# Kernel tuning notes

Measured on AMD Instinct MI355X. Metric: run time of the kernel, lower is better.

## Reference

```python
import jax, jax.numpy as jnp
import numpy as np

B, H, S, D = 2, 16, 2048, 64


def setup_inputs() -> dict:
    key = jax.random.key(0)
    kq, kk, kv = jax.random.split(key, 3)
    q = jax.random.normal(kq, (B, H, S, D), dtype=jnp.float32)
    k = jax.random.normal(kk, (B, H, S, D), dtype=jnp.float32)
    v = jax.random.normal(kv, (B, H, S, D), dtype=jnp.float32)
    # causal mask: 1.0 where attention is DISALLOWED (strictly upper triangle)
    mask = jnp.triu(jnp.ones((S, S), dtype=jnp.float32), k=1)[None, None, :, :]
    return {"k": k, "q": q, "v": v, "mask": mask}


def reference(k, q, v, mask):
    d_k = jnp.asarray(k.shape[-1], dtype=jnp.float32)
    # scores: [B, H, S, S]
    scores = jnp.einsum("bhqd,bhkd->bhqk", q, k) / jnp.sqrt(d_k)
    scores = scores + mask * (-1e9)
    weights = jax.nn.softmax(scores, axis=-1)
    # attention output: [B, H, S, D]
    return jnp.einsum("bhqk,bhkd->bhqd", weights, v)
```

## Files before the change

kernel.cpp:

```cpp
#include <hip/hip_runtime.h>
#include <hip/hip_bf16.h>

typedef unsigned short ushort_t;
typedef __attribute__((ext_vector_type(8))) short v8s;
typedef __attribute__((ext_vector_type(4))) float v4f;

#define SEQ   2048
#define DH    64
#define NHEAD 32
#define BK    32
#define NQT32 64
#define KSTR  72
#define VSTR  40

__device__ __forceinline__ unsigned pkbf(float lo, float hi) {
    __hip_bfloat162 h = __float22bfloat162_rn(make_float2(lo, hi));
    union { __hip_bfloat162 h; unsigned u; } c; c.h = h; return c.u;
}

__device__ __forceinline__ v8s load8_bf_scaled(const float* p, float sc) {
    float4 a = *(const float4*)p;
    float4 b = *(const float4*)(p + 4);
    union { v8s v; unsigned u[4]; } t;
    t.u[0] = pkbf(a.x * sc, a.y * sc);
    t.u[1] = pkbf(a.z * sc, a.w * sc);
    t.u[2] = pkbf(b.x * sc, b.y * sc);
    t.u[3] = pkbf(b.z * sc, b.w * sc);
    return t.v;
}

__device__ __forceinline__ void stage_store(ushort_t* kdst, ushort_t* vdst,
                                            float4 k0, float4 k1,
                                            const float* va, const float* vb) {
    union { v8s v; unsigned u[4]; } kc, vc;
    kc.u[0] = pkbf(k0.x, k0.y); kc.u[1] = pkbf(k0.z, k0.w);
    kc.u[2] = pkbf(k1.x, k1.y); kc.u[3] = pkbf(k1.z, k1.w);
    vc.u[0] = pkbf(va[0], vb[0]); vc.u[1] = pkbf(va[1], vb[1]);
    vc.u[2] = pkbf(va[2], vb[2]); vc.u[3] = pkbf(va[3], vb[3]);
    *(v8s*)kdst = kc.v;
    *(v8s*)vdst = vc.v;
}

__global__ __launch_bounds__(256, 4)
void attn_causal_kernel(const float* __restrict__ Kg,
                        const float* __restrict__ Qg,
                        const float* __restrict__ Vg,
                        float* __restrict__ Og) {
    __shared__ alignas(16) ushort_t Kt[2][BK * KSTR];
    __shared__ alignas(16) ushort_t Vt[2][DH * VSTR];
    __shared__ alignas(16) ushort_t Pb[4][16 * VSTR];

    const int i    = blockIdx.x;
    const int head = i & 31;
    const int pair = i >> 5;
    const int qbL  = pair * 32;
    const int qbH  = (NQT32 - 1 - pair) * 32;
    const int tid  = threadIdx.x;
    const int wv   = tid >> 6;
    const int lane = tid & 63;
    const int l15  = lane & 15;
    const int quad = lane >> 4;

    const int myq0 = (wv < 2) ? (qbL + wv * 16) : (qbH + (wv - 2) * 16);
    const int qmax = myq0 + 15;

    const size_t hb = (size_t)head * SEQ * DH;

    v8s qa0, qa1;
    {
        const float* qp = Qg + hb + (size_t)(myq0 + l15) * DH + quad * 8;
        qa0 = load8_bf_scaled(qp, 0.125f);
        qa1 = load8_bf_scaled(qp + 32, 0.125f);
    }

    v4f a0 = {0.f,0.f,0.f,0.f}, a1 = a0, a2 = a0, a3 = a0;
    float lsum[4] = {0.f,0.f,0.f,0.f};

    const int ntiles = NQT32 - pair;

    const int sk_kpos = tid >> 3;
    const int sk_d    = (tid & 7) * 8;
    const int sv_d = tid & 63;

    const float* kbase  = Kg + hb + (size_t)sk_kpos * DH + sk_d;
    const float* vbaseA = Vg + hb + (size_t)(4 * wv) * DH + sv_d;
    const float* vbaseB = Vg + hb + (size_t)(16 + 4 * wv) * DH + sv_d;
    ushort_t* kdst0 = &Kt[0][sk_kpos * KSTR + sk_d];
    ushort_t* vdst0 = &Vt[0][sv_d * VSTR + wv * 8];
    const int kofs = BK * KSTR;
    const int vofs = DH * VSTR;

    {
        float4 k0 = *(const float4*)(kbase);
        float4 k1 = *(const float4*)(kbase + 4);
        float va[4], vb[4];
        #pragma unroll
        for (int m = 0; m < 4; ++m) {
            va[m] = vbaseA[(size_t)m * DH];
            vb[m] = vbaseB[(size_t)m * DH];
        }
        stage_store(kdst0, vdst0, k0, k1, va, vb);
    }
    __syncthreads();

    for (int kt = 0; kt < ntiles; ++kt) {
        const int cur = kt & 1;
        const bool havenext = (kt + 1 < ntiles);

        float4 nk0, nk1; float nva[4], nvb[4];
        if (havenext) {
            const size_t toff = (size_t)(kt + 1) * BK * DH;
            nk0 = *(const float4*)(kbase + toff);
            nk1 = *(const float4*)(kbase + toff + 4);
            #pragma unroll
            for (int m = 0; m < 4; ++m) {
                nva[m] = vbaseA[toff + (size_t)m * DH];
                nvb[m] = vbaseB[toff + (size_t)m * DH];
            }
        }

        const int kb = kt * BK;
        if (kb <= qmax) {
            const ushort_t* KB = &Kt[0][cur ? kofs : 0];
            const ushort_t* VB = &Vt[0][cur ? vofs : 0];
            union { v8s v; uint4 u; } k00, k01, k10, k11, vb0, vb1, vb2, vb3;
            k00.u = *(const uint4*)&KB[(l15)      * KSTR      + quad * 8];
            k01.u = *(const uint4*)&KB[(l15)      * KSTR + 32 + quad * 8];
            k10.u = *(const uint4*)&KB[(16 + l15) * KSTR      + quad * 8];
            k11.u = *(const uint4*)&KB[(16 + l15) * KSTR + 32 + quad * 8];
            vb0.u = *(const uint4*)&VB[(l15)      * VSTR + quad * 8];
            vb1.u = *(const uint4*)&VB[(16 + l15) * VSTR + quad * 8];
            vb2.u = *(const uint4*)&VB[(32 + l15) * VSTR + quad * 8];
            vb3.u = *(const uint4*)&VB[(48 + l15) * VSTR + quad * 8];

            const v4f z = {0.f, 0.f, 0.f, 0.f};
            v4f c0 = __builtin_amdgcn_mfma_f32_16x16x32_bf16(qa0, k00.v, z, 0, 0, 0);
            c0     = __builtin_amdgcn_mfma_f32_16x16x32_bf16(qa1, k01.v, c0, 0, 0, 0);
            v4f c1 = __builtin_amdgcn_mfma_f32_16x16x32_bf16(qa0, k10.v, z, 0, 0, 0);
            c1     = __builtin_amdgcn_mfma_f32_16x16x32_bf16(qa1, k11.v, c1, 0, 0, 0);

            float p0[4], p1[4];
            if (kb + BK <= myq0) {
                #pragma unroll
                for (int r = 0; r < 4; ++r) { p0[r] = __expf(c0[r]); p1[r] = __expf(c1[r]); }
            } else {
                #pragma unroll
                for (int r = 0; r < 4; ++r) {
                    const int rg = myq0 + quad * 4 + r;
                    p0[r] = (kb + l15      <= rg) ? __expf(c0[r]) : 0.f;
                    p1[r] = (kb + 16 + l15 <= rg) ? __expf(c1[r]) : 0.f;
                }
            }
            ushort_t* PW = &Pb[wv][0];
            #pragma unroll
            for (int r = 0; r < 4; ++r) {
                lsum[r] += p0[r] + p1[r];
                *(unsigned*)&PW[(quad * 4 + r) * VSTR + 2 * l15] = pkbf(p0[r], p1[r]);
            }
            union { v8s v; uint4 u; } pa;
            pa.u = *(const uint4*)&PW[l15 * VSTR + quad * 8];
            a0 = __builtin_amdgcn_mfma_f32_16x16x32_bf16(pa.v, vb0.v, a0, 0, 0, 0);
            a1 = __builtin_amdgcn_mfma_f32_16x16x32_bf16(pa.v, vb1.v, a1, 0, 0, 0);
            a2 = __builtin_amdgcn_mfma_f32_16x16x32_bf16(pa.v, vb2.v, a2, 0, 0, 0);
            a3 = __builtin_amdgcn_mfma_f32_16x16x32_bf16(pa.v, vb3.v, a3, 0, 0, 0);
        }

        if (havenext) {
            const int nxt = cur ^ 1;
            stage_store(kdst0 + (nxt ? kofs : 0), vdst0 + (nxt ? vofs : 0),
                        nk0, nk1, nva, nvb);
        }

        __syncthreads();
    }

    #pragma unroll
    for (int off = 1; off < 16; off <<= 1) {
        #pragma unroll
        for (int r = 0; r < 4; ++r)
            lsum[r] += __shfl_xor(lsum[r], off);
    }
    #pragma unroll
    for (int r = 0; r < 4; ++r) {
        const float inv = 1.0f / lsum[r];
        float* op = Og + hb + (size_t)(myq0 + quad * 4 + r) * DH + l15;
        op[0]  = a0[r] * inv;
        op[16] = a1[r] * inv;
        op[32] = a2[r] * inv;
        op[48] = a3[r] * inv;
    }
}

extern "C" void kernel_launch(void* const* d_in, const int* in_sizes, int n_in,
                              void* d_out, int out_size, void* d_ws, size_t ws_size,
                              hipStream_t stream) {
    const float* K = (const float*)d_in[0];
    const float* Q = (const float*)d_in[1];
    const float* V = (const float*)d_in[2];
    float* O = (float*)d_out;
    attn_causal_kernel<<<dim3(1024), 256, 0, stream>>>(K, Q, V, O);
}
```

Baseline: 145.3 us.

## Transpose QK^T MFMA to keep P in registers and split KV tiles across two wave groups

Computes S^T with K as the A operand, so the probabilities come out in the layout needed for the PV MFMA and the LDS round-trip for P goes away. Each block now has 512 threads in two groups that take alternating KV tiles. Each wave handles both a low and a high 16-row query slice, reusing each staged K/V tile twice. Partial accumulators and row sums are merged through LDS at the end. This halves the grid, raises register pressure from the doubled accumulators, and adds extra syncs for the merge.

```diff
diff --git a/kernel.cpp b/kernel.cpp
--- a/kernel.cpp
+++ b/kernel.cpp
@@ -9,9 +9,9 @@
 #define DH    64
 #define NHEAD 32
 #define BK    32
-#define NQT32 64
 #define KSTR  72
 #define VSTR  40
+#define MSTR  20
 
 __device__ __forceinline__ unsigned pkbf(float lo, float hi) {
     __hip_bfloat162 h = __float22bfloat162_rn(make_float2(lo, hi));
@@ -29,87 +29,123 @@
     return t.v;
 }
 
-__device__ __forceinline__ void stage_store(ushort_t* kdst, ushort_t* vdst,
-                                            float4 k0, float4 k1,
-                                            const float* va, const float* vb) {
-    union { v8s v; unsigned u[4]; } kc, vc;
-    kc.u[0] = pkbf(k0.x, k0.y); kc.u[1] = pkbf(k0.z, k0.w);
-    kc.u[2] = pkbf(k1.x, k1.y); kc.u[3] = pkbf(k1.z, k1.w);
-    vc.u[0] = pkbf(va[0], vb[0]); vc.u[1] = pkbf(va[1], vb[1]);
-    vc.u[2] = pkbf(va[2], vb[2]); vc.u[3] = pkbf(va[3], vb[3]);
-    *(v8s*)kdst = kc.v;
-    *(v8s*)vdst = vc.v;
-}
-
-__global__ __launch_bounds__(256, 4)
+__device__ __forceinline__ void process_tile_T(
+    int kb, int myq0, int quad, int l15,
+    v8s qa0, v8s qa1,
+    v8s ka00, v8s ka01, v8s ka10, v8s ka11,
+    v8s vb0, v8s vb1, v8s vb2, v8s vb3,
+    v4f& a0, v4f& a1, v4f& a2, v4f& a3, float& ls)
+{
+    const v4f z = {0.f, 0.f, 0.f, 0.f};
+    v4f s0 = __builtin_amdgcn_mfma_f32_16x16x32_bf16(ka00, qa0, z, 0, 0, 0);
+    s0     = __builtin_amdgcn_mfma_f32_16x16x32_bf16(ka01, qa1, s0, 0, 0, 0);
+    v4f s1 = __builtin_amdgcn_mfma_f32_16x16x32_bf16(ka10, qa0, z, 0, 0, 0);
+    s1     = __builtin_amdgcn_mfma_f32_16x16x32_bf16(ka11, qa1, s1, 0, 0, 0);
+
+    float p0[4], p1[4];
+    if (kb + BK <= myq0) {
+        #pragma unroll
+        for (int r = 0; r < 4; ++r) { p0[r] = __expf(s0[r]); p1[r] = __expf(s1[r]); }
+    } else {
+        const int qrow = myq0 + l15;
+        #pragma unroll
+        for (int r = 0; r < 4; ++r) {
+            p0[r] = (kb + 4 * quad + r      <= qrow) ? __expf(s0[r]) : 0.f;
+            p1[r] = (kb + 16 + 4 * quad + r <= qrow) ? __expf(s1[r]) : 0.f;
+        }
+    }
+    #pragma unroll
+    for (int r = 0; r < 4; ++r) ls += p0[r] + p1[r];
+
+    union { v8s v; unsigned u[4]; } pa;
+    pa.u[0] = pkbf(p0[0], p0[1]); pa.u[1] = pkbf(p0[2], p0[3]);
+    pa.u[2] = pkbf(p1[0], p1[1]); pa.u[3] = pkbf(p1[2], p1[3]);
+    a0 = __builtin_amdgcn_mfma_f32_16x16x32_bf16(pa.v, vb0, a0, 0, 0, 0);
+    a1 = __builtin_amdgcn_mfma_f32_16x16x32_bf16(pa.v, vb1, a1, 0, 0, 0);
+    a2 = __builtin_amdgcn_mfma_f32_16x16x32_bf16(pa.v, vb2, a2, 0, 0, 0);
+    a3 = __builtin_amdgcn_mfma_f32_16x16x32_bf16(pa.v, vb3, a3, 0, 0, 0);
+}
+
+__global__ __launch_bounds__(512, 4)
 void attn_causal_kernel(const float* __restrict__ Kg,
                         const float* __restrict__ Qg,
                         const float* __restrict__ Vg,
                         float* __restrict__ Og) {
-    __shared__ alignas(16) ushort_t Kt[2][BK * KSTR];
-    __shared__ alignas(16) ushort_t Vt[2][DH * VSTR];
-    __shared__ alignas(16) ushort_t Pb[4][16 * VSTR];
+    __shared__ alignas(16) ushort_t Kt[2][2][BK * KSTR];
+    __shared__ alignas(16) ushort_t Vt[2][2][DH * VSTR];
+    __shared__ alignas(16) float    Macc[4][64][MSTR];
+    __shared__ float                Mls[4][16];
 
     const int i    = blockIdx.x;
     const int head = i & 31;
-    const int pair = i >> 5;
-    const int qbL  = pair * 32;
-    const int qbH  = (NQT32 - 1 - pair) * 32;
+    const int p    = i >> 5;
+    const int qbL  = p * 64;
+    const int qbH  = (31 - p) * 64;
     const int tid  = threadIdx.x;
-    const int wv   = tid >> 6;
+    const int grp  = tid >> 8;
+    const int gtid = tid & 255;
+    const int gw   = gtid >> 6;
     const int lane = tid & 63;
     const int l15  = lane & 15;
     const int quad = lane >> 4;
 
-    const int myq0 = (wv < 2) ? (qbL + wv * 16) : (qbH + (wv - 2) * 16);
-    const int qmax = myq0 + 15;
-
+    const int myq0L = qbL + gw * 16, qmaxL = myq0L + 15;
+    const int myq0H = qbH + gw * 16, qmaxH = myq0H + 15;
     const size_t hb = (size_t)head * SEQ * DH;
 
-    v8s qa0, qa1;
+    v8s qaL0, qaL1, qaH0, qaH1;
     {
-        const float* qp = Qg + hb + (size_t)(myq0 + l15) * DH + quad * 8;
-        qa0 = load8_bf_scaled(qp, 0.125f);
-        qa1 = load8_bf_scaled(qp + 32, 0.125f);
-    }
-
-    v4f a0 = {0.f,0.f,0.f,0.f}, a1 = a0, a2 = a0, a3 = a0;
-    float lsum[4] = {0.f,0.f,0.f,0.f};
-
-    const int ntiles = NQT32 - pair;
-
-    const int sk_kpos = tid >> 3;
-    const int sk_d    = (tid & 7) * 8;
-    const int sv_d = tid & 63;
+        const float* qpL = Qg + hb + (size_t)(myq0L + l15) * DH + quad * 8;
+        const float* qpH = Qg + hb + (size_t)(myq0H + l15) * DH + quad * 8;
+        qaL0 = load8_bf_scaled(qpL, 0.125f);  qaL1 = load8_bf_scaled(qpL + 32, 0.125f);
+        qaH0 = load8_bf_scaled(qpH, 0.125f);  qaH1 = load8_bf_scaled(qpH + 32, 0.125f);
+    }
+
+    v4f aL0 = {0.f,0.f,0.f,0.f}, aL1 = aL0, aL2 = aL0, aL3 = aL0;
+    v4f aH0 = aL0, aH1 = aL0, aH2 = aL0, aH3 = aL0;
+    float lsL = 0.f, lsH = 0.f;
+
+    const int nt = 32 - p;
+
+    const int sk_kpos = gtid >> 3;
+    const int sk_d    = (gtid & 7) * 8;
+    const int sv_d = gtid & 63;
 
     const float* kbase  = Kg + hb + (size_t)sk_kpos * DH + sk_d;
-    const float* vbaseA = Vg + hb + (size_t)(4 * wv) * DH + sv_d;
-    const float* vbaseB = Vg + hb + (size_t)(16 + 4 * wv) * DH + sv_d;
-    ushort_t* kdst0 = &Kt[0][sk_kpos * KSTR + sk_d];
-    ushort_t* vdst0 = &Vt[0][sv_d * VSTR + wv * 8];
-    const int kofs = BK * KSTR;
-    const int vofs = DH * VSTR;
+    const float* vbaseA = Vg + hb + (size_t)(4 * gw) * DH + sv_d;
+    const float* vbaseB = Vg + hb + (size_t)(16 + 4 * gw) * DH + sv_d;
+    ushort_t* kdst0 = &Kt[grp][0][sk_kpos * KSTR + sk_d];
+    ushort_t* vdst0 = &Vt[grp][0][sv_d * VSTR + 8 * gw];
+    const int KOFS = BK * KSTR;
+    const int VOFS = DH * VSTR;
 
     {
-        float4 k0 = *(const float4*)(kbase);
-        float4 k1 = *(const float4*)(kbase + 4);
+        const size_t toff = (size_t)grp * BK * DH;
+        float4 k0 = *(const float4*)(kbase + toff);
+        float4 k1 = *(const float4*)(kbase + toff + 4);
         float va[4], vb[4];
         #pragma unroll
         for (int m = 0; m < 4; ++m) {
-            va[m] = vbaseA[(size_t)m * DH];
-            vb[m] = vbaseB[(size_t)m * DH];
-        }
-        stage_store(kdst0, vdst0, k0, k1, va, vb);
-    }
-    __syncthreads();
-
-    for (int kt = 0; kt < ntiles; ++kt) {
-        const int cur = kt & 1;
-        const bool havenext = (kt + 1 < ntiles);
+            va[m] = vbaseA[toff + (size_t)m * DH];
+            vb[m] = vbaseB[toff + (size_t)m * DH];
+        }
+        union { v8s v; unsigned u[4]; } kc, vc;
+        kc.u[0] = pkbf(k0.x, k0.y); kc.u[1] = pkbf(k0.z, k0.w);
+        kc.u[2] = pkbf(k1.x, k1.y); kc.u[3] = pkbf(k1.z, k1.w);
+        vc.u[0] = pkbf(va[0], va[1]); vc.u[1] = pkbf(va[2], va[3]);
+        vc.u[2] = pkbf(vb[0], vb[1]); vc.u[3] = pkbf(vb[2], vb[3]);
+        *(v8s*)kdst0 = kc.v;
+        *(v8s*)vdst0 = vc.v;
+    }
+    __syncthreads();
+
+    for (int t = 0; t < nt; ++t) {
+        const int cur = t & 1;
+        const bool havenext = (t + 1 < nt);
 
         float4 nk0, nk1; float nva[4], nvb[4];
         if (havenext) {
-            const size_t toff = (size_t)(kt + 1) * BK * DH;
+            const size_t toff = (size_t)(2 * (t + 1) + grp) * BK * DH;
             nk0 = *(const float4*)(kbase + toff);
             nk1 = *(const float4*)(kbase + toff + 4);
             #pragma unroll
@@ -119,75 +155,89 @@
             }
         }
 
-        const int kb = kt * BK;
-        if (kb <= qmax) {
-            const ushort_t* KB = &Kt[0][cur ? kofs : 0];
-            const ushort_t* VB = &Vt[0][cur ? vofs : 0];
-            union { v8s v; uint4 u; } k00, k01, k10, k11, vb0, vb1, vb2, vb3;
-            k00.u = *(const uint4*)&KB[(l15)      * KSTR      + quad * 8];
-            k01.u = *(const uint4*)&KB[(l15)      * KSTR + 32 + quad * 8];
-            k10.u = *(const uint4*)&KB[(16 + l15) * KSTR      + quad * 8];
-            k11.u = *(const uint4*)&KB[(16 + l15) * KSTR + 32 + quad * 8];
-            vb0.u = *(const uint4*)&VB[(l15)      * VSTR + quad * 8];
-            vb1.u = *(const uint4*)&VB[(16 + l15) * VSTR + quad * 8];
-            vb2.u = *(const uint4*)&VB[(32 + l15) * VSTR + quad * 8];
-            vb3.u = *(const uint4*)&VB[(48 + l15) * VSTR + quad * 8];
-
-            const v4f z = {0.f, 0.f, 0.f, 0.f};
-            v4f c0 = __builtin_amdgcn_mfma_f32_16x16x32_bf16(qa0, k00.v, z, 0, 0, 0);
-            c0     = __builtin_amdgcn_mfma_f32_16x16x32_bf16(qa1, k01.v, c0, 0, 0, 0);
-            v4f c1 = __builtin_amdgcn_mfma_f32_16x16x32_bf16(qa0, k10.v, z, 0, 0, 0);
-            c1     = __builtin_amdgcn_mfma_f32_16x16x32_bf16(qa1, k11.v, c1, 0, 0, 0);
-
-            float p0[4], p1[4];
-            if (kb + BK <= myq0) {
-                #pragma unroll
-                for (int r = 0; r < 4; ++r) { p0[r] = __expf(c0[r]); p1[r] = __expf(c1[r]); }
-            } else {
-                #pragma unroll
-                for (int r = 0; r < 4; ++r) {
-                    const int rg = myq0 + quad * 4 + r;
-                    p0[r] = (kb + l15      <= rg) ? __expf(c0[r]) : 0.f;
-                    p1[r] = (kb + 16 + l15 <= rg) ? __expf(c1[r]) : 0.f;
-                }
-            }
-            ushort_t* PW = &Pb[wv][0];
-            #pragma unroll
-            for (int r = 0; r < 4; ++r) {
-                lsum[r] += p0[r] + p1[r];
-                *(unsigned*)&PW[(quad * 4 + r) * VSTR + 2 * l15] = pkbf(p0[r], p1[r]);
-            }
-            union { v8s v; uint4 u; } pa;
-            pa.u = *(const uint4*)&PW[l15 * VSTR + quad * 8];
-            a0 = __builtin_amdgcn_mfma_f32_16x16x32_bf16(pa.v, vb0.v, a0, 0, 0, 0);
-            a1 = __builtin_amdgcn_mfma_f32_16x16x32_bf16(pa.v, vb1.v, a1, 0, 0, 0);
-            a2 = __builtin_amdgcn_mfma_f32_16x16x32_bf16(pa.v, vb2.v, a2, 0, 0, 0);
-            a3 = __builtin_amdgcn_mfma_f32_16x16x32_bf16(pa.v, vb3.v, a3, 0, 0, 0);
+        const int kb = (2 * t + grp) * BK;
+        if (kb <= qmaxL || kb <= qmaxH) {
+            const ushort_t* KB = &Kt[grp][0][cur ? KOFS : 0];
+            const ushort_t* VB = &Vt[grp][0][cur ? VOFS : 0];
+            union { v8s v; uint4 u; } ka00, ka01, ka10, ka11, vb0, vb1, vb2, vb3;
+            ka00.u = *(const uint4*)&KB[(l15)      * KSTR      + quad * 8];
+            ka01.u = *(const uint4*)&KB[(l15)      * KSTR + 32 + quad * 8];
+            ka10.u = *(const uint4*)&KB[(16 + l15) * KSTR      + quad * 8];
+            ka11.u = *(const uint4*)&KB[(16 + l15) * KSTR + 32 + quad * 8];
+            vb0.u  = *(const uint4*)&VB[(l15)      * VSTR + quad * 8];
+            vb1.u  = *(const uint4*)&VB[(16 + l15) * VSTR + quad * 8];
+            vb2.u  = *(const uint4*)&VB[(32 + l15) * VSTR + quad * 8];
+            vb3.u  = *(const uint4*)&VB[(48 + l15) * VSTR + quad * 8];
+
+            if (kb <= qmaxL)
+                process_tile_T(kb, myq0L, quad, l15, qaL0, qaL1,
+                               ka00.v, ka01.v, ka10.v, ka11.v,
+                               vb0.v, vb1.v, vb2.v, vb3.v,
+                               aL0, aL1, aL2, aL3, lsL);
+            if (kb <= qmaxH)
+                process_tile_T(kb, myq0H, quad, l15, qaH0, qaH1,
+                               ka00.v, ka01.v, ka10.v, ka11.v,
+                               vb0.v, vb1.v, vb2.v, vb3.v,
+                               aH0, aH1, aH2, aH3, lsH);
         }
 
         if (havenext) {
+            union { v8s v; unsigned u[4]; } kc, vc;
+            kc.u[0] = pkbf(nk0.x, nk0.y); kc.u[1] = pkbf(nk0.z, nk0.w);
+            kc.u[2] = pkbf(nk1.x, nk1.y); kc.u[3] = pkbf(nk1.z, nk1.w);
+            vc.u[0] = pkbf(nva[0], nva[1]); vc.u[1] = pkbf(nva[2], nva[3]);
+            vc.u[2] = pkbf(nvb[0], nvb[1]); vc.u[3] = pkbf(nvb[2], nvb[3]);
             const int nxt = cur ^ 1;
-            stage_store(kdst0 + (nxt ? kofs : 0), vdst0 + (nxt ? vofs : 0),
-                        nk0, nk1, nva, nvb);
+            *(v8s*)(kdst0 + (nxt ? KOFS : 0)) = kc.v;
+            *(v8s*)(vdst0 + (nxt ? VOFS : 0)) = vc.v;
         }
 
         __syncthreads();
     }
 
-    #pragma unroll
-    for (int off = 1; off < 16; off <<= 1) {
-        #pragma unroll
-        for (int r = 0; r < 4; ++r)
-            lsum[r] += __shfl_xor(lsum[r], off);
-    }
-    #pragma unroll
-    for (int r = 0; r < 4; ++r) {
-        const float inv = 1.0f / lsum[r];
-        float* op = Og + hb + (size_t)(myq0 + quad * 4 + r) * DH + l15;
-        op[0]  = a0[r] * inv;
-        op[16] = a1[r] * inv;
-        op[32] = a2[r] * inv;
-        op[48] = a3[r] * inv;
+    lsL += __shfl_xor(lsL, 16); lsL += __shfl_xor(lsL, 32);
+    lsH += __shfl_xor(lsH, 16); lsH += __shfl_xor(lsH, 32);
+
+    if (grp == 1) {
+        float* d = &Macc[gw][lane][0];
+        *(v4f*)(d + 0) = aL0; *(v4f*)(d + 4) = aL1;
+        *(v4f*)(d + 8) = aL2; *(v4f*)(d + 12) = aL3;
+        if (lane < 16) Mls[gw][lane] = lsL;
+    }
+    __syncthreads();
+    if (grp == 0) {
+        const float* s = &Macc[gw][lane][0];
+        aL0 += *(const v4f*)(s + 0); aL1 += *(const v4f*)(s + 4);
+        aL2 += *(const v4f*)(s + 8); aL3 += *(const v4f*)(s + 12);
+        const float lt = lsL + Mls[gw][l15];
+        #pragma unroll
+        for (int r = 0; r < 4; ++r) {
+            const float inv = 1.0f / __shfl(lt, 4 * quad + r);
+            float* op = Og + hb + (size_t)(myq0L + 4 * quad + r) * DH + l15;
+            op[0]  = aL0[r] * inv; op[16] = aL1[r] * inv;
+            op[32] = aL2[r] * inv; op[48] = aL3[r] * inv;
+        }
+    }
+    __syncthreads();
+    if (grp == 1) {
+        float* d = &Macc[gw][lane][0];
+        *(v4f*)(d + 0) = aH0; *(v4f*)(d + 4) = aH1;
+        *(v4f*)(d + 8) = aH2; *(v4f*)(d + 12) = aH3;
+        if (lane < 16) Mls[gw][lane] = lsH;
+    }
+    __syncthreads();
+    if (grp == 0) {
+        const float* s = &Macc[gw][lane][0];
+        aH0 += *(const v4f*)(s + 0); aH1 += *(const v4f*)(s + 4);
+        aH2 += *(const v4f*)(s + 8); aH3 += *(const v4f*)(s + 12);
+        const float lt = lsH + Mls[gw][l15];
+        #pragma unroll
+        for (int r = 0; r < 4; ++r) {
+            const float inv = 1.0f / __shfl(lt, 4 * quad + r);
+            float* op = Og + hb + (size_t)(myq0H + 4 * quad + r) * DH + l15;
+            op[0]  = aH0[r] * inv; op[16] = aH1[r] * inv;
+            op[32] = aH2[r] * inv; op[48] = aH3[r] * inv;
+        }
     }
 }
 
@@ -198,5 +248,5 @@
     const float* Q = (const float*)d_in[1];
     const float* V = (const float*)d_in[2];
     float* O = (float*)d_out;
-    attn_causal_kernel<<<dim3(1024), 256, 0, stream>>>(K, Q, V, O);
-}
+    attn_causal_kernel<<<dim3(512), 512, 0, stream>>>(K, Q, V, O);
+}
```

Measured after the change: 173.2 us. 19.1% more time.
